# Optimization experiments

Measured on AMD Instinct MI355X. Metric: run time of the kernel, lower is better.

The kernel has to match this reference:

```python
import jax, jax.numpy as jnp
import numpy as np

NNODES = 8192
DIM = 64
K = 32
ALPHA = 3.0


def setup_inputs() -> dict:
    key = jax.random.key(0)
    ks = jax.random.split(key, 7)
    idx = jnp.arange(NNODES, dtype=jnp.int64)
    # xavier_uniform for 2D params, uniform[0,1) for biases (per _reset_parameters)
    def xavier(k, shape):
        fan_in, fan_out = shape[1], shape[0]
        bound = float(np.sqrt(6.0 / (fan_in + fan_out)))
        return jax.random.uniform(k, shape, jnp.float32, -bound, bound)
    E1 = xavier(ks[0], (NNODES, DIM))
    E2 = xavier(ks[1], (NNODES, DIM))
    W1 = xavier(ks[2], (DIM, DIM))
    b1 = jax.random.uniform(ks[3], (DIM,), jnp.float32)
    W2 = xavier(ks[4], (DIM, DIM))
    b2 = jax.random.uniform(ks[5], (DIM,), jnp.float32)
    return {"idx": idx, "E1": E1, "E2": E2, "W1": W1, "b1": b1, "W2": W2, "b2": b2}


def reference(idx, E1, E2, W1, b1, W2, b2):
    n = idx.shape[0]
    # embedding lookups [n, dim]
    v1 = E1[idx]
    v2 = E2[idx]
    # linear (torch: x @ W.T + b) then tanh saturation
    v1 = jnp.tanh(ALPHA * (v1 @ W1.T + b1))
    v2 = jnp.tanh(ALPHA * (v2 @ W2.T + b2))
    # antisymmetric score matrix [n, n]
    a = v1 @ v2.T - v2 @ v1.T
    A = jax.nn.relu(jnp.tanh(ALPHA * a))
    # top-k per row -> binary mask via scatter
    _, t1 = jax.lax.top_k(A, K)  # [n, K]
    rows = jnp.arange(n)[:, None]
    mask = jnp.zeros((n, n), A.dtype).at[rows, t1].set(1.0)
    return A * mask
```

## Files before the change

kernel.cpp:

```cpp
#include <hip/hip_runtime.h>
#include <stdint.h>
#include <math.h>

#define NN 8192
#define DIM 64
#define KSEL 32
#define BK2 16
#define TILE 128
#define NTB (NN / TILE)
#define NTRI ((NTB * (NTB + 1)) / 2)

#define AS1 __attribute__((address_space(1)))
#define AS3 __attribute__((address_space(3)))

__device__ __forceinline__ float tanh_xla(float x) {
    const float kClamp = 7.90531110763549805f;
    float xc = fminf(fmaxf(x, -kClamp), kClamp);
    float x2 = xc * xc;
    float p = -2.76076847742355e-16f;
    p = fmaf(x2, p, 2.00018790482477e-13f);
    p = fmaf(x2, p, -8.60467152213735e-11f);
    p = fmaf(x2, p, 5.12229709037114e-08f);
    p = fmaf(x2, p, 1.48572235717979e-05f);
    p = fmaf(x2, p, 6.37261928875436e-04f);
    p = fmaf(x2, p, 4.89352455891786e-03f);
    p = xc * p;
    float q = 1.19825839466702e-06f;
    q = fmaf(x2, q, 1.18534705686654e-04f);
    q = fmaf(x2, q, 2.26843463243900e-03f);
    q = fmaf(x2, q, 4.89352518554385e-03f);
    float r = p / q;
    return (fabsf(x) < 0.0004f) ? x : r;
}
__device__ __forceinline__ float tanh_xla_pos(float ax) {
    const float kClamp = 7.90531110763549805f;
    float xc = fminf(ax, kClamp);
    float x2 = xc * xc;
    float p = -2.76076847742355e-16f;
    p = fmaf(x2, p, 2.00018790482477e-13f);
    p = fmaf(x2, p, -8.60467152213735e-11f);
    p = fmaf(x2, p, 5.12229709037114e-08f);
    p = fmaf(x2, p, 1.48572235717979e-05f);
    p = fmaf(x2, p, 6.37261928875436e-04f);
    p = fmaf(x2, p, 4.89352455891786e-03f);
    p = xc * p;
    float q = 1.19825839466702e-06f;
    q = fmaf(x2, q, 1.18534705686654e-04f);
    q = fmaf(x2, q, 2.26843463243900e-03f);
    q = fmaf(x2, q, 4.89352518554385e-03f);
    float r = p / q;
    return (ax < 0.0004f) ? ax : r;
}

__global__ __launch_bounds__(256) void k_embed(
    const int* __restrict__ gidx,
    const float* __restrict__ E1, const float* __restrict__ E2,
    const float* __restrict__ W1, const float* __restrict__ b1,
    const float* __restrict__ W2, const float* __restrict__ b2,
    float* __restrict__ VT1, float* __restrict__ VT2)
{
    __shared__ float W1s[DIM][DIM + 1];
    __shared__ float W2s[DIM][DIM + 1];
    __shared__ float E1s[4][DIM];
    __shared__ float E2s[4][DIM];
    __shared__ float T1[DIM][5];
    __shared__ float T2[DIM][5];
    const int t = threadIdx.x;
    for (int i = t; i < DIM * DIM; i += 256) {
        W1s[i >> 6][i & 63] = W1[i];
        W2s[i >> 6][i & 63] = W2[i];
    }
    const int rbase = blockIdx.x * 4;
    for (int i = t; i < 4 * DIM; i += 256) {
        const int r = i >> 6, k = i & 63;
        const int g = gidx[rbase + r];
        E1s[r][k] = E1[(size_t)g * DIM + k];
        E2s[r][k] = E2[(size_t)g * DIM + k];
    }
    __syncthreads();
    const int o = t & 63, rs = t >> 6;
    float m1 = 0.0f, m2 = 0.0f;
    #pragma unroll
    for (int k = 0; k < DIM; ++k) {
        m1 = fmaf(E1s[rs][k], W1s[o][k], m1);
        m2 = fmaf(E2s[rs][k], W2s[o][k], m2);
    }
    T1[o][rs] = tanh_xla(3.0f * (m1 + b1[o]));
    T2[o][rs] = tanh_xla(3.0f * (m2 + b2[o]));
    __syncthreads();
    const int oo = t >> 2, rr = t & 3;
    VT1[(size_t)oo * NN + rbase + rr] = T1[oo][rr];
    VT2[(size_t)oo * NN + rbase + rr] = T2[oo][rr];
}

__global__ __launch_bounds__(256) void k_score(
    const float* __restrict__ VT1, const float* __restrict__ VT2,
    float* __restrict__ out)
{
    const int L = blockIdx.x;
    int bi = (int)(64.5f - sqrtf(fmaf(-2.0f, (float)L, 64.5f * 64.5f)));
    while (bi * NTB - (bi * (bi - 1)) / 2 > L) --bi;
    while ((bi + 1) * NTB - ((bi + 1) * bi) / 2 <= L) ++bi;
    const int bj = bi + (L - (bi * NTB - (bi * (bi - 1)) / 2));

    __shared__ __align__(16) float lds[2][4][BK2][TILE];

    const int t = threadIdx.x;
    const int tx = t & 15;
    const int ty = t >> 4;
    const int Ibase = bi * TILE, Jbase = bj * TILE;

    const int w = t >> 6, l = t & 63;
    const float* vt = (w & 1) ? VT2 : VT1;
    const int cbase = (w & 2) ? Jbase : Ibase;
    const int srow = (l >> 5);
    const int scol = (l & 31) * 4;

    float acc1[8][8], acc2[8][8];
    #pragma unroll
    for (int i = 0; i < 8; ++i)
        #pragma unroll
        for (int j = 0; j < 8; ++j) { acc1[i][j] = 0.0f; acc2[i][j] = 0.0f; }

    #pragma unroll
    for (int p = 0; p < 8; ++p) {
        const float* src = vt + (size_t)(2 * p + srow) * NN + cbase + scol;
        __builtin_amdgcn_global_load_lds((AS1 const void*)src,
                                         (AS3 void*)&lds[0][w][2 * p + srow][scol], 16, 0, 0);
    }
    __syncthreads();

    for (int c4 = 0; c4 < 4; ++c4) {
        const int cur = c4 & 1;
        if (c4 < 3) {
            const int ckn = (c4 + 1) * BK2;
            #pragma unroll
            for (int p = 0; p < 8; ++p) {
                const float* src = vt + (size_t)(ckn + 2 * p + srow) * NN + cbase + scol;
                __builtin_amdgcn_global_load_lds((AS1 const void*)src,
                                                 (AS3 void*)&lds[cur ^ 1][w][2 * p + srow][scol], 16, 0, 0);
            }
        }
        #pragma unroll 2
        for (int k = 0; k < BK2; ++k) {
            float a1[8], a2[8], c1[8], c2[8];
            *(float4*)&a1[0] = *(const float4*)&lds[cur][0][k][ty * 8];
            *(float4*)&a1[4] = *(const float4*)&lds[cur][0][k][ty * 8 + 4];
            *(float4*)&a2[0] = *(const float4*)&lds[cur][1][k][ty * 8];
            *(float4*)&a2[4] = *(const float4*)&lds[cur][1][k][ty * 8 + 4];
            *(float4*)&c1[0] = *(const float4*)&lds[cur][2][k][tx * 4];
            *(float4*)&c1[4] = *(const float4*)&lds[cur][2][k][tx * 4 + 64];
            *(float4*)&c2[0] = *(const float4*)&lds[cur][3][k][tx * 4];
            *(float4*)&c2[4] = *(const float4*)&lds[cur][3][k][tx * 4 + 64];
            #pragma unroll
            for (int i = 0; i < 8; ++i)
                #pragma unroll
                for (int j = 0; j < 8; ++j) {
                    acc1[i][j] = fmaf(a1[i], c2[j], acc1[i][j]);
                    acc2[i][j] = fmaf(a2[i], c1[j], acc2[i][j]);
                }
        }
        __syncthreads();
    }

    #pragma unroll
    for (int i = 0; i < 8; ++i)
        #pragma unroll
        for (int j = 0; j < 8; ++j) {
            const float aa = acc1[i][j] - acc2[i][j];
            const float tt = tanh_xla_pos(3.0f * fabsf(aa));
            acc1[i][j] = (aa > 0.0f) ? tt : 0.0f;
            acc2[i][j] = (aa < 0.0f) ? tt : 0.0f;
        }
    #pragma unroll
    for (int i = 0; i < 8; ++i) {
        const int gi = Ibase + ty * 8 + i;
        *(float4*)&out[(size_t)gi * NN + Jbase + tx * 4] =
            make_float4(acc1[i][0], acc1[i][1], acc1[i][2], acc1[i][3]);
        *(float4*)&out[(size_t)gi * NN + Jbase + 64 + tx * 4] =
            make_float4(acc1[i][4], acc1[i][5], acc1[i][6], acc1[i][7]);
    }
    if (bi != bj) {
        #pragma unroll
        for (int j = 0; j < 8; ++j) {
            const int gj = Jbase + tx * 4 + (j >> 2) * 64 + (j & 3);
            float4* p = (float4*)&out[(size_t)gj * NN + Ibase + ty * 8];
            p[0] = make_float4(acc2[0][j], acc2[1][j], acc2[2][j], acc2[3][j]);
            p[1] = make_float4(acc2[4][j], acc2[5][j], acc2[6][j], acc2[7][j]);
        }
    }
}

__global__ __launch_bounds__(256) void k_topk(float* __restrict__ out)
{
    __shared__ uint32_t hist[2048];
    __shared__ uint32_t waveTot[4];
    __shared__ uint32_t redm[4];
    __shared__ uint32_t segTot[4][8];
    __shared__ int xstar_s;
    __shared__ uint32_t bc_bin, bc_ca, bc_m, bc_flag;

    const int row = blockIdx.x;
    const int t = threadIdx.x;
    const int wid = t >> 6, lane = t & 63;
    float* rp = out + (size_t)row * NN;

    float v[32];
    #pragma unroll
    for (int s = 0; s < 8; ++s) {
        const float4 f = *(const float4*)&rp[(s * 256 + t) * 4];
        v[s*4+0] = f.x; v[s*4+1] = f.y; v[s*4+2] = f.z; v[s*4+3] = f.w;
    }
    if (t == 0) bc_flag = 0;

    const uint32_t Cb = __float_as_uint(tanh_xla_pos(8.0f));

    uint32_t isC = 0, maxv = 0;
    #pragma unroll
    for (int s = 0; s < 8; ++s)
        #pragma unroll
        for (int e = 0; e < 4; ++e) {
            const uint32_t vb = __float_as_uint(v[s*4+e]);
            if (vb == Cb) isC |= (1u << (s * 4 + e));
            maxv = vb > maxv ? vb : maxv;
        }
    {
        uint32_t s01 = (uint32_t)__popc(isC & 0x0000000Fu) | ((uint32_t)__popc(isC & 0x000000F0u) << 16);
        uint32_t s23 = (uint32_t)__popc(isC & 0x00000F00u) | ((uint32_t)__popc(isC & 0x0000F000u) << 16);
        uint32_t s45 = (uint32_t)__popc(isC & 0x000F0000u) | ((uint32_t)__popc(isC & 0x00F00000u) << 16);
        uint32_t s67 = (uint32_t)__popc(isC & 0x0F000000u) | ((uint32_t)__popc(isC & 0xF0000000u) << 16);
        uint32_t m = maxv;
        #pragma unroll
        for (int d = 1; d < 64; d <<= 1) {
            s01 += (uint32_t)__shfl_down((int)s01, d, 64);
            s23 += (uint32_t)__shfl_down((int)s23, d, 64);
            s45 += (uint32_t)__shfl_down((int)s45, d, 64);
            s67 += (uint32_t)__shfl_down((int)s67, d, 64);
            const uint32_t om = (uint32_t)__shfl_down((int)m, d, 64);
            m = om > m ? om : m;
        }
        if (lane == 0) {
            segTot[wid][0] = s01 & 0xFFFFu; segTot[wid][1] = s01 >> 16;
            segTot[wid][2] = s23 & 0xFFFFu; segTot[wid][3] = s23 >> 16;
            segTot[wid][4] = s45 & 0xFFFFu; segTot[wid][5] = s45 >> 16;
            segTot[wid][6] = s67 & 0xFFFFu; segTot[wid][7] = s67 >> 16;
            redm[wid] = m;
        }
    }
    __syncthreads();
    uint32_t segSum[8]; uint32_t cntC = 0;
    #pragma unroll
    for (int s = 0; s < 8; ++s) {
        segSum[s] = segTot[0][s] + segTot[1][s] + segTot[2][s] + segTot[3][s];
        cntC += segSum[s];
    }
    uint32_t mAll = redm[0];
    mAll = redm[1] > mAll ? redm[1] : mAll;
    mAll = redm[2] > mAll ? redm[2] : mAll;
    mAll = redm[3] > mAll ? redm[3] : mAll;
    __syncthreads();

    if (mAll == Cb && cntC >= (uint32_t)KSEL) {
        uint32_t acc = 0; int sstar = 7;
        #pragma unroll
        for (int s = 0; s < 8; ++s) {
            if (acc + segSum[s] >= (uint32_t)KSEL && acc < (uint32_t)KSEL) { sstar = s; break; }
            acc += segSum[s];
        }
        const uint32_t need2 = (uint32_t)KSEL - acc;
        const uint32_t nib = (isC >> (sstar * 4)) & 0xFu;
        uint32_t cs = (uint32_t)__popc(nib);
        uint32_t inc = cs;
        #pragma unroll
        for (int d = 1; d < 64; d <<= 1) {
            const uint32_t o = (uint32_t)__shfl_up((int)inc, d, 64);
            if (lane >= d) inc += o;
        }
        if (lane == 63) waveTot[wid] = inc;
        __syncthreads();
        uint32_t woff = 0;
        for (int w2 = 0; w2 < wid; ++w2) woff += waveTot[w2];
        const uint32_t pre = woff + inc - cs;
        if (pre < need2 && need2 <= pre + cs) {
            uint32_t nn = need2 - pre, mm = nib; int bit = 0;
            for (uint32_t q2 = 0; q2 < nn; ++q2) { bit = __ffs(mm) - 1; mm &= mm - 1u; }
            xstar_s = sstar * 1024 + t * 4 + bit;
        }
        __syncthreads();
        const int xs = xstar_s;
        #pragma unroll
        for (int s = 0; s < 8; ++s) {
            float w2[4];
            #pragma unroll
            for (int e = 0; e < 4; ++e) {
                const float a = v[s*4+e];
                const int gi = s * 1024 + t * 4 + e;
                w2[e] = (__float_as_uint(a) == Cb && gi <= xs) ? a : 0.f;
            }
            *(float4*)&rp[(s * 256 + t) * 4] = make_float4(w2[0], w2[1], w2[2], w2[3]);
        }
        return;
    }

    uint64_t prefix = 0, thr = 0;
    int need = KSEL;
    bool done = false;

    for (int pass = 0; pass < 4; ++pass) {
        const int shift = 33 - 11 * pass;
        {
            const uint4 z = make_uint4(0u, 0u, 0u, 0u);
            uint4* hp = (uint4*)hist;
            hp[t] = z; hp[256 + t] = z;
        }
        __syncthreads();
        #pragma unroll
        for (int s = 0; s < 8; ++s) {
            #pragma unroll
            for (int e = 0; e < 4; ++e) {
                const uint32_t vb = __float_as_uint(v[s*4+e]);
                if (vb == 0u) continue;
                const int gi = s * 1024 + t * 4 + e;
                const uint64_t key = ((uint64_t)vb << 13) | (uint32_t)(8191 - gi);
                if ((key >> (shift + 11)) == prefix)
                    atomicAdd(&hist[(uint32_t)((key >> shift) & 2047u)], 1u);
            }
        }
        __syncthreads();
        uint32_t m[8]; uint32_t tot = 0;
        #pragma unroll
        for (int i = 0; i < 8; ++i) {
            m[i] = hist[t * 8 + i];
            tot += m[i];
        }
        uint32_t ssum = tot;
        #pragma unroll
        for (int d = 1; d < 64; d <<= 1) {
            const uint32_t o = __shfl_down(ssum, d, 64);
            if (lane + d < 64) ssum += o;
        }
        if (lane == 0) waveTot[wid] = ssum;
        __syncthreads();
        {
            uint32_t above = 0;
            for (int w2 = wid + 1; w2 < 4; ++w2) above += waveTot[w2];
            if (pass == 0) {
                const uint32_t totalAll = waveTot[0] + waveTot[1] + waveTot[2] + waveTot[3];
                if (totalAll < (uint32_t)need && t == 0) bc_flag = 1;
            }
            uint32_t c = (ssum - tot) + above;
            #pragma unroll
            for (int i = 7; i >= 0; --i) {
                if (c < (uint32_t)need && (uint32_t)need <= c + m[i]) {
                    bc_bin = (uint32_t)(t * 8 + i);
                    bc_ca  = c;
                    bc_m   = m[i];
                }
                c += m[i];
            }
        }
        __syncthreads();
        if (bc_flag) { thr = 1; done = true; }
        else {
            prefix = (prefix << 11) | (uint64_t)bc_bin;
            need  -= (int)bc_ca;
            if ((uint32_t)need == bc_m) {
                thr = prefix << shift;
                done = true;
            } else if (pass == 3) { thr = prefix; done = true; }
        }
        if (done) break;
        __syncthreads();
    }

    #pragma unroll
    for (int s = 0; s < 8; ++s) {
        float w[4];
        #pragma unroll
        for (int e = 0; e < 4; ++e) {
            const float a = v[s*4+e];
            const uint32_t vb = __float_as_uint(a);
            const int gi = s * 1024 + t * 4 + e;
            const uint64_t key = ((uint64_t)vb << 13) | (uint32_t)(8191 - gi);
            w[e] = (vb != 0u && key >= thr) ? a : 0.f;
        }
        *(float4*)&rp[(s * 256 + t) * 4] = make_float4(w[0], w[1], w[2], w[3]);
    }
}

extern "C" void kernel_launch(void* const* d_in, const int* in_sizes, int n_in,
                              void* d_out, int out_size, void* d_ws, size_t ws_size,
                              hipStream_t stream)
{
    const int*   idx = (const int*)  d_in[0];
    const float* E1  = (const float*)d_in[1];
    const float* E2  = (const float*)d_in[2];
    const float* W1  = (const float*)d_in[3];
    const float* b1  = (const float*)d_in[4];
    const float* W2  = (const float*)d_in[5];
    const float* b2  = (const float*)d_in[6];
    float* out = (float*)d_out;
    float* VT1 = (float*)d_ws;
    float* VT2 = VT1 + (size_t)NN * DIM;

    k_embed<<<NN / 4, 256, 0, stream>>>(idx, E1, E2, W1, b1, W2, b2, VT1, VT2);
    k_score<<<NTRI, 256, 0, stream>>>(VT1, VT2, out);
    k_topk<<<NN, 256, 0, stream>>>(out);
}
```

Measured before the change: 286.3 us.

## Split score tile's two GEMMs across two 256-thread groups and exchange via LDS

The score kernel now launches 512 threads per block. Each half computes one of the two products (v1·v2ᵀ or v2·v1ᵀ) with a single 8x8 accumulator instead of two. Group 1 passes its partial results through shared memory to group 0, which does the subtraction, the tanh and both stores. The aim is to halve per-thread register pressure and double the waves available for latency hiding. In exchange it adds an extra barrier and LDS round trip, and half the threads sit idle during the epilogue and stores.

After: 294.2 us. 1.03x slower.

```diff
diff --git a/kernel.cpp b/kernel.cpp
--- a/kernel.cpp
+++ b/kernel.cpp
@@ -93,7 +93,7 @@
     VT2[(size_t)oo * NN + rbase + rr] = T2[oo][rr];
 }
 
-__global__ __launch_bounds__(256) void k_score(
+__global__ __launch_bounds__(512) void k_score(
     const float* __restrict__ VT1, const float* __restrict__ VT2,
     float* __restrict__ out)
 {
@@ -104,89 +104,102 @@
     const int bj = bi + (L - (bi * NTB - (bi * (bi - 1)) / 2));
 
     __shared__ __align__(16) float lds[2][4][BK2][TILE];
+    float* ex = &lds[0][0][0][0];
 
     const int t = threadIdx.x;
-    const int tx = t & 15;
-    const int ty = t >> 4;
+    const int grp = t >> 8;
+    const int tg = t & 255;
+    const int tx = tg & 15;
+    const int ty = tg >> 4;
     const int Ibase = bi * TILE, Jbase = bj * TILE;
 
     const int w = t >> 6, l = t & 63;
-    const float* vt = (w & 1) ? VT2 : VT1;
-    const int cbase = (w & 2) ? Jbase : Ibase;
-    const int srow = (l >> 5);
+    const int sa = w & 3;
+    const float* vt = (sa & 1) ? VT2 : VT1;
+    const int cbase = (sa & 2) ? Jbase : Ibase;
+    const int rhalf = (w >> 2) * 8;
+    const int srow = rhalf + (l >> 5);
     const int scol = (l & 31) * 4;
 
-    float acc1[8][8], acc2[8][8];
+    float acc[8][8];
     #pragma unroll
     for (int i = 0; i < 8; ++i)
         #pragma unroll
-        for (int j = 0; j < 8; ++j) { acc1[i][j] = 0.0f; acc2[i][j] = 0.0f; }
-
-    #pragma unroll
-    for (int p = 0; p < 8; ++p) {
+        for (int j = 0; j < 8; ++j) acc[i][j] = 0.0f;
+
+    #pragma unroll
+    for (int p = 0; p < 4; ++p) {
         const float* src = vt + (size_t)(2 * p + srow) * NN + cbase + scol;
         __builtin_amdgcn_global_load_lds((AS1 const void*)src,
-                                         (AS3 void*)&lds[0][w][2 * p + srow][scol], 16, 0, 0);
-    }
-    __syncthreads();
+                                         (AS3 void*)&lds[0][sa][2 * p + srow][scol], 16, 0, 0);
+    }
+    __syncthreads();
+
+    const int aArr = grp ? 1 : 0;
+    const int cArr = grp ? 2 : 3;
 
     for (int c4 = 0; c4 < 4; ++c4) {
         const int cur = c4 & 1;
         if (c4 < 3) {
             const int ckn = (c4 + 1) * BK2;
             #pragma unroll
-            for (int p = 0; p < 8; ++p) {
+            for (int p = 0; p < 4; ++p) {
                 const float* src = vt + (size_t)(ckn + 2 * p + srow) * NN + cbase + scol;
                 __builtin_amdgcn_global_load_lds((AS1 const void*)src,
-                                                 (AS3 void*)&lds[cur ^ 1][w][2 * p + srow][scol], 16, 0, 0);
+                                                 (AS3 void*)&lds[cur ^ 1][sa][2 * p + srow][scol], 16, 0, 0);
             }
         }
         #pragma unroll 2
         for (int k = 0; k < BK2; ++k) {
-            float a1[8], a2[8], c1[8], c2[8];
-            *(float4*)&a1[0] = *(const float4*)&lds[cur][0][k][ty * 8];
-            *(float4*)&a1[4] = *(const float4*)&lds[cur][0][k][ty * 8 + 4];
-            *(float4*)&a2[0] = *(const float4*)&lds[cur][1][k][ty * 8];
-            *(float4*)&a2[4] = *(const float4*)&lds[cur][1][k][ty * 8 + 4];
-            *(float4*)&c1[0] = *(const float4*)&lds[cur][2][k][tx * 4];
-            *(float4*)&c1[4] = *(const float4*)&lds[cur][2][k][tx * 4 + 64];
-            *(float4*)&c2[0] = *(const float4*)&lds[cur][3][k][tx * 4];
-            *(float4*)&c2[4] = *(const float4*)&lds[cur][3][k][tx * 4 + 64];
+            float a[8], c[8];
+            *(float4*)&a[0] = *(const float4*)&lds[cur][aArr][k][ty * 8];
+            *(float4*)&a[4] = *(const float4*)&lds[cur][aArr][k][ty * 8 + 4];
+            *(float4*)&c[0] = *(const float4*)&lds[cur][cArr][k][tx * 4];
+            *(float4*)&c[4] = *(const float4*)&lds[cur][cArr][k][tx * 4 + 64];
             #pragma unroll
             for (int i = 0; i < 8; ++i)
                 #pragma unroll
-                for (int j = 0; j < 8; ++j) {
-                    acc1[i][j] = fmaf(a1[i], c2[j], acc1[i][j]);
-                    acc2[i][j] = fmaf(a2[i], c1[j], acc2[i][j]);
-                }
-        }
-        __syncthreads();
-    }
-
-    #pragma unroll
-    for (int i = 0; i < 8; ++i)
-        #pragma unroll
-        for (int j = 0; j < 8; ++j) {
-            const float aa = acc1[i][j] - acc2[i][j];
-            const float tt = tanh_xla_pos(3.0f * fabsf(aa));
-            acc1[i][j] = (aa > 0.0f) ? tt : 0.0f;
-            acc2[i][j] = (aa < 0.0f) ? tt : 0.0f;
-        }
-    #pragma unroll
-    for (int i = 0; i < 8; ++i) {
-        const int gi = Ibase + ty * 8 + i;
-        *(float4*)&out[(size_t)gi * NN + Jbase + tx * 4] =
-            make_float4(acc1[i][0], acc1[i][1], acc1[i][2], acc1[i][3]);
-        *(float4*)&out[(size_t)gi * NN + Jbase + 64 + tx * 4] =
-            make_float4(acc1[i][4], acc1[i][5], acc1[i][6], acc1[i][7]);
-    }
-    if (bi != bj) {
-        #pragma unroll
-        for (int j = 0; j < 8; ++j) {
-            const int gj = Jbase + tx * 4 + (j >> 2) * 64 + (j & 3);
-            float4* p = (float4*)&out[(size_t)gj * NN + Ibase + ty * 8];
-            p[0] = make_float4(acc2[0][j], acc2[1][j], acc2[2][j], acc2[3][j]);
-            p[1] = make_float4(acc2[4][j], acc2[5][j], acc2[6][j], acc2[7][j]);
+                for (int j = 0; j < 8; ++j)
+                    acc[i][j] = fmaf(a[i], c[j], acc[i][j]);
+        }
+        __syncthreads();
+    }
+
+    if (grp == 1) {
+        #pragma unroll
+        for (int q = 0; q < 16; ++q) {
+            const int i = q >> 1, j4 = (q & 1) * 4;
+            ((float4*)ex)[q * 256 + tg] =
+                make_float4(acc[i][j4], acc[i][j4 + 1], acc[i][j4 + 2], acc[i][j4 + 3]);
+        }
+    }
+    __syncthreads();
+    if (grp == 0) {
+        #pragma unroll
+        for (int q = 0; q < 16; ++q) {
+            const int i = q >> 1, j4 = (q & 1) * 4;
+            const float4 f4 = ((float4*)ex)[q * 256 + tg];
+            float wn[4];
+            const float m2v[4] = {f4.x, f4.y, f4.z, f4.w};
+            #pragma unroll
+            for (int e = 0; e < 4; ++e) {
+                const float aa = acc[i][j4 + e] - m2v[e];
+                const float tt = tanh_xla_pos(3.0f * fabsf(aa));
+                wn[e] = (aa > 0.0f) ? tt : 0.0f;
+                acc[i][j4 + e] = (aa < 0.0f) ? tt : 0.0f;
+            }
+            const int gi = Ibase + ty * 8 + i;
+            *(float4*)&out[(size_t)gi * NN + Jbase + (q & 1) * 64 + tx * 4] =
+                make_float4(wn[0], wn[1], wn[2], wn[3]);
+        }
+        if (bi != bj) {
+            #pragma unroll
+            for (int j = 0; j < 8; ++j) {
+                const int gj = Jbase + tx * 4 + (j >> 2) * 64 + (j & 3);
+                float4* p = (float4*)&out[(size_t)gj * NN + Ibase + ty * 8];
+                p[0] = make_float4(acc[0][j], acc[1][j], acc[2][j], acc[3][j]);
+                p[1] = make_float4(acc[4][j], acc[5][j], acc[6][j], acc[7][j]);
+            }
         }
     }
 }
@@ -404,6 +417,6 @@
     float* VT2 = VT1 + (size_t)NN * DIM;
 
     k_embed<<<NN / 4, 256, 0, stream>>>(idx, E1, E2, W1, b1, W2, b2, VT1, VT2);
-    k_score<<<NTRI, 256, 0, stream>>>(VT1, VT2, out);
+    k_score<<<NTRI, 512, 0, stream>>>(VT1, VT2, out);
     k_topk<<<NN, 256, 0, stream>>>(out);
 }
```

## Add global max-saturation flag so top-k scans row chunks and exits early

Applied to the files above, without the earlier changes.

k_score now computes the per-tile maximum and sets a global violation flag when any value exceeds the saturated tanh constant. When the flag is clear, k_topk reads the row one 1024-element chunk at a time, counts saturated entries with a prefix scan, and stops reading once 32 are found. It then writes the selected constants and zeros the remaining chunks. This avoids loading the full row and running the histogram radix select. The cost is an atomic per score block, a global read per top-k block, and extra barriers per chunk.

Result: slower. 365.7 us (+27.7%).

```diff
diff --git a/kernel.cpp b/kernel.cpp
--- a/kernel.cpp
+++ b/kernel.cpp
@@ -57,7 +57,8 @@
     const float* __restrict__ E1, const float* __restrict__ E2,
     const float* __restrict__ W1, const float* __restrict__ b1,
     const float* __restrict__ W2, const float* __restrict__ b2,
-    float* __restrict__ VT1, float* __restrict__ VT2)
+    float* __restrict__ VT1, float* __restrict__ VT2,
+    uint32_t* __restrict__ viol)
 {
     __shared__ float W1s[DIM][DIM + 1];
     __shared__ float W2s[DIM][DIM + 1];
@@ -66,6 +67,7 @@
     __shared__ float T1[DIM][5];
     __shared__ float T2[DIM][5];
     const int t = threadIdx.x;
+    if (blockIdx.x == 0 && t == 0) *viol = 0u;
     for (int i = t; i < DIM * DIM; i += 256) {
         W1s[i >> 6][i & 63] = W1[i];
         W2s[i >> 6][i & 63] = W2[i];
@@ -95,7 +97,7 @@
 
 __global__ __launch_bounds__(256) void k_score(
     const float* __restrict__ VT1, const float* __restrict__ VT2,
-    float* __restrict__ out)
+    float* __restrict__ out, uint32_t* __restrict__ viol)
 {
     const int L = blockIdx.x;
     int bi = (int)(64.5f - sqrtf(fmaf(-2.0f, (float)L, 64.5f * 64.5f)));
@@ -163,6 +165,8 @@
         __syncthreads();
     }
 
+    const uint32_t Cb = __float_as_uint(tanh_xla_pos(8.0f));
+    uint32_t mx = 0;
     #pragma unroll
     for (int i = 0; i < 8; ++i)
         #pragma unroll
@@ -171,7 +175,12 @@
             const float tt = tanh_xla_pos(3.0f * fabsf(aa));
             acc1[i][j] = (aa > 0.0f) ? tt : 0.0f;
             acc2[i][j] = (aa < 0.0f) ? tt : 0.0f;
-        }
+            const uint32_t u1 = __float_as_uint(acc1[i][j]);
+            const uint32_t u2 = __float_as_uint(acc2[i][j]);
+            mx = u1 > mx ? u1 : mx;
+            mx = u2 > mx ? u2 : mx;
+        }
+    if (mx > Cb) atomicOr(viol, 1u);
     #pragma unroll
     for (int i = 0; i < 8; ++i) {
         const int gi = Ibase + ty * 8 + i;
@@ -191,19 +200,78 @@
     }
 }
 
-__global__ __launch_bounds__(256) void k_topk(float* __restrict__ out)
+__global__ __launch_bounds__(256) void k_topk(float* __restrict__ out,
+                                              const uint32_t* __restrict__ viol)
 {
     __shared__ uint32_t hist[2048];
     __shared__ uint32_t waveTot[4];
-    __shared__ uint32_t redm[4];
-    __shared__ uint32_t segTot[4][8];
-    __shared__ int xstar_s;
+    __shared__ int xs_s;
     __shared__ uint32_t bc_bin, bc_ca, bc_m, bc_flag;
 
     const int row = blockIdx.x;
     const int t = threadIdx.x;
     const int wid = t >> 6, lane = t & 63;
     float* rp = out + (size_t)row * NN;
+    const uint32_t Cb = __float_as_uint(tanh_xla_pos(8.0f));
+    const float Cf = __uint_as_float(Cb);
+
+    if (*viol == 0u) {
+        uint32_t kb = 0;
+        int found = 0;
+        int mchunk = -1;
+        for (int ch = 0; ch < 8; ++ch) {
+            const float4 f = *(const float4*)&rp[ch * 1024 + t * 4];
+            uint32_t nib = 0;
+            if (__float_as_uint(f.x) == Cb) nib |= 1u;
+            if (__float_as_uint(f.y) == Cb) nib |= 2u;
+            if (__float_as_uint(f.z) == Cb) nib |= 4u;
+            if (__float_as_uint(f.w) == Cb) nib |= 8u;
+            kb |= nib << (ch * 4);
+            const uint32_t c = (uint32_t)__popc(nib);
+            uint32_t inc = c;
+            #pragma unroll
+            for (int d = 1; d < 64; d <<= 1) {
+                const uint32_t o = (uint32_t)__shfl_up((int)inc, d, 64);
+                if (lane >= d) inc += o;
+            }
+            if (lane == 63) waveTot[wid] = inc;
+            __syncthreads();
+            const int tot = (int)(waveTot[0] + waveTot[1] + waveTot[2] + waveTot[3]);
+            if (found + tot >= KSEL) {
+                const uint32_t need2 = (uint32_t)(KSEL - found);
+                uint32_t woff = 0;
+                for (int w2 = 0; w2 < wid; ++w2) woff += waveTot[w2];
+                const uint32_t pre = woff + inc - c;
+                if (pre < need2 && need2 <= pre + c) {
+                    uint32_t nn = need2 - pre, mm = nib; int bit = 0;
+                    for (uint32_t q2 = 0; q2 < nn; ++q2) { bit = __ffs(mm) - 1; mm &= mm - 1u; }
+                    xs_s = ch * 1024 + t * 4 + bit;
+                }
+                __syncthreads();
+                mchunk = ch;
+                break;
+            }
+            found += tot;
+            __syncthreads();
+        }
+        if (mchunk >= 0) {
+            const int xs = xs_s;
+            for (int ch = 0; ch <= mchunk; ++ch) {
+                const uint32_t nib = (kb >> (ch * 4)) & 0xFu;
+                float w[4];
+                #pragma unroll
+                for (int e = 0; e < 4; ++e) {
+                    const int gi = ch * 1024 + t * 4 + e;
+                    w[e] = (((nib >> e) & 1u) && gi <= xs) ? Cf : 0.0f;
+                }
+                *(float4*)&rp[ch * 1024 + t * 4] = make_float4(w[0], w[1], w[2], w[3]);
+            }
+            const float4 z4 = make_float4(0.f, 0.f, 0.f, 0.f);
+            for (int ch = mchunk + 1; ch < 8; ++ch)
+                *(float4*)&rp[ch * 1024 + t * 4] = z4;
+            return;
+        }
+    }
 
     float v[32];
     #pragma unroll
@@ -212,95 +280,7 @@
         v[s*4+0] = f.x; v[s*4+1] = f.y; v[s*4+2] = f.z; v[s*4+3] = f.w;
     }
     if (t == 0) bc_flag = 0;
-
-    const uint32_t Cb = __float_as_uint(tanh_xla_pos(8.0f));
-
-    uint32_t isC = 0, maxv = 0;
-    #pragma unroll
-    for (int s = 0; s < 8; ++s)
-        #pragma unroll
-        for (int e = 0; e < 4; ++e) {
-            const uint32_t vb = __float_as_uint(v[s*4+e]);
-            if (vb == Cb) isC |= (1u << (s * 4 + e));
-            maxv = vb > maxv ? vb : maxv;
-        }
-    {
-        uint32_t s01 = (uint32_t)__popc(isC & 0x0000000Fu) | ((uint32_t)__popc(isC & 0x000000F0u) << 16);
-        uint32_t s23 = (uint32_t)__popc(isC & 0x00000F00u) | ((uint32_t)__popc(isC & 0x0000F000u) << 16);
-        uint32_t s45 = (uint32_t)__popc(isC & 0x000F0000u) | ((uint32_t)__popc(isC & 0x00F00000u) << 16);
-        uint32_t s67 = (uint32_t)__popc(isC & 0x0F000000u) | ((uint32_t)__popc(isC & 0xF0000000u) << 16);
-        uint32_t m = maxv;
-        #pragma unroll
-        for (int d = 1; d < 64; d <<= 1) {
-            s01 += (uint32_t)__shfl_down((int)s01, d, 64);
-            s23 += (uint32_t)__shfl_down((int)s23, d, 64);
-            s45 += (uint32_t)__shfl_down((int)s45, d, 64);
-            s67 += (uint32_t)__shfl_down((int)s67, d, 64);
-            const uint32_t om = (uint32_t)__shfl_down((int)m, d, 64);
-            m = om > m ? om : m;
-        }
-        if (lane == 0) {
-            segTot[wid][0] = s01 & 0xFFFFu; segTot[wid][1] = s01 >> 16;
-            segTot[wid][2] = s23 & 0xFFFFu; segTot[wid][3] = s23 >> 16;
-            segTot[wid][4] = s45 & 0xFFFFu; segTot[wid][5] = s45 >> 16;
-            segTot[wid][6] = s67 & 0xFFFFu; segTot[wid][7] = s67 >> 16;
-            redm[wid] = m;
-        }
-    }
     __syncthreads();
-    uint32_t segSum[8]; uint32_t cntC = 0;
-    #pragma unroll
-    for (int s = 0; s < 8; ++s) {
-        segSum[s] = segTot[0][s] + segTot[1][s] + segTot[2][s] + segTot[3][s];
-        cntC += segSum[s];
-    }
-    uint32_t mAll = redm[0];
-    mAll = redm[1] > mAll ? redm[1] : mAll;
-    mAll = redm[2] > mAll ? redm[2] : mAll;
-    mAll = redm[3] > mAll ? redm[3] : mAll;
-    __syncthreads();
-
-    if (mAll == Cb && cntC >= (uint32_t)KSEL) {
-        uint32_t acc = 0; int sstar = 7;
-        #pragma unroll
-        for (int s = 0; s < 8; ++s) {
-            if (acc + segSum[s] >= (uint32_t)KSEL && acc < (uint32_t)KSEL) { sstar = s; break; }
-            acc += segSum[s];
-        }
-        const uint32_t need2 = (uint32_t)KSEL - acc;
-        const uint32_t nib = (isC >> (sstar * 4)) & 0xFu;
-        uint32_t cs = (uint32_t)__popc(nib);
-        uint32_t inc = cs;
-        #pragma unroll
-        for (int d = 1; d < 64; d <<= 1) {
-            const uint32_t o = (uint32_t)__shfl_up((int)inc, d, 64);
-            if (lane >= d) inc += o;
-        }
-        if (lane == 63) waveTot[wid] = inc;
-        __syncthreads();
-        uint32_t woff = 0;
-        for (int w2 = 0; w2 < wid; ++w2) woff += waveTot[w2];
-        const uint32_t pre = woff + inc - cs;
-        if (pre < need2 && need2 <= pre + cs) {
-            uint32_t nn = need2 - pre, mm = nib; int bit = 0;
-            for (uint32_t q2 = 0; q2 < nn; ++q2) { bit = __ffs(mm) - 1; mm &= mm - 1u; }
-            xstar_s = sstar * 1024 + t * 4 + bit;
-        }
-        __syncthreads();
-        const int xs = xstar_s;
-        #pragma unroll
-        for (int s = 0; s < 8; ++s) {
-            float w2[4];
-            #pragma unroll
-            for (int e = 0; e < 4; ++e) {
-                const float a = v[s*4+e];
-                const int gi = s * 1024 + t * 4 + e;
-                w2[e] = (__float_as_uint(a) == Cb && gi <= xs) ? a : 0.f;
-            }
-            *(float4*)&rp[(s * 256 + t) * 4] = make_float4(w2[0], w2[1], w2[2], w2[3]);
-        }
-        return;
-    }
 
     uint64_t prefix = 0, thr = 0;
     int need = KSEL;
@@ -402,8 +382,9 @@
     float* out = (float*)d_out;
     float* VT1 = (float*)d_ws;
     float* VT2 = VT1 + (size_t)NN * DIM;
-
-    k_embed<<<NN / 4, 256, 0, stream>>>(idx, E1, E2, W1, b1, W2, b2, VT1, VT2);
-    k_score<<<NTRI, 256, 0, stream>>>(VT1, VT2, out);
-    k_topk<<<NN, 256, 0, stream>>>(out);
-}
+    uint32_t* viol = (uint32_t*)(VT2 + (size_t)NN * DIM);
+
+    k_embed<<<NN / 4, 256, 0, stream>>>(idx, E1, E2, W1, b1, W2, b2, VT1, VT2, viol);
+    k_score<<<NTRI, 256, 0, stream>>>(VT1, VT2, out, viol);
+    k_topk<<<NN, 256, 0, stream>>>(out, viol);
+}
```
